# Performance work log

Measured on AMD Instinct MI355X. Metric: run time of the kernel, lower is better.

The kernel has to match this reference:

```python
import jax, jax.numpy as jnp
import numpy as np

B, D, H, C = 131072, 256, 256, 8
TAU = 0.15


def setup_inputs() -> dict:
    key = jax.random.key(0)
    ks = jax.random.split(key, 10)
    s_in = 1.0 / np.sqrt(D)
    s_h = 1.0 / np.sqrt(H)
    return {
        "x": jax.random.normal(ks[0], (B, D), jnp.float32),
        # root node params
        "W1": jax.random.normal(ks[1], (D, H), jnp.float32) * s_in,
        "b1": jnp.zeros((H,), jnp.float32),
        "W2": jax.random.normal(ks[2], (H, C), jnp.float32) * s_h,
        "b2": jnp.zeros((C,), jnp.float32),
        # one leaf child per class: stacked params [C, ...]
        "Wc1": jax.random.normal(ks[3], (C, H, H), jnp.float32) * s_h,
        "bc1": jnp.zeros((C, H), jnp.float32),
        "Wc2": jax.random.normal(ks[4], (C, H, C), jnp.float32) * s_h,
        "bc2": jnp.zeros((C, C), jnp.float32),
        "tau": jnp.full((C,), TAU, jnp.float32),
    }


def reference(x, W1, b1, W2, b2, Wc1, bc1, Wc2, bc2, tau):
    # root dense + head
    h = jax.nn.relu(x @ W1 + b1)            # [B, H]
    logits = h @ W2 + b2                    # [B, C]
    probs = jax.nn.softmax(logits, axis=1)  # [B, C]

    # route(): walk classes in descending prob order, take the first class
    # that has a child (all C do here) and whose prob >= tau[class].
    # Equivalent vectorized form: argmax of probs restricted to passing classes.
    mask = probs >= tau                     # [B, C]
    routed = jnp.any(mask, axis=1)          # [B]
    masked = jnp.where(mask, probs, -1.0)
    best = jnp.argmax(masked, axis=1)       # [B] chosen child per sample

    out_logits, out_h = logits, h
    for c in range(C):                      # small fixed expert loop
        sel = (routed & (best == c))[:, None]
        h_c = jax.nn.relu(h @ Wc1[c] + bc1[c])  # [B, H]
        l_c = h_c @ Wc2[c] + bc2[c]             # [B, C]
        out_logits = jnp.where(sel, l_c, out_logits)
        out_h = jnp.where(sel, h_c, out_h)

    depths = routed.astype(jnp.int32)       # leaf children => depth 1, else 0
    return out_logits, out_h, depths
```

## Files before the change

kernel.cpp:

```cpp
#include <hip/hip_runtime.h>

#define Bn 131072
#define Dn 256
#define Hn 256
#define Cn 8

typedef __attribute__((ext_vector_type(4))) float f32x4;
typedef __attribute__((ext_vector_type(8))) __bf16 bf16x8;

#define LDA 40

__device__ inline unsigned short rtn_bf16(float v) {
    unsigned int u = __float_as_uint(v);
    unsigned int r = u + 0x7fffu + ((u >> 16) & 1u);
    return (unsigned short)(r >> 16);
}
__device__ inline float bf16_to_f(unsigned short h) {
    return __uint_as_float((unsigned int)h << 16);
}
__device__ inline void split3(float v, unsigned short& a0, unsigned short& a1,
                              unsigned short& a2) {
    a0 = rtn_bf16(v); float r = v - bf16_to_f(a0);
    a1 = rtn_bf16(r); r -= bf16_to_f(a1);
    a2 = rtn_bf16(r);
}
__device__ inline void split2(float v, unsigned short& a0, unsigned short& a1) {
    a0 = rtn_bf16(v);
    a1 = rtn_bf16(v - bf16_to_f(a0));
}

__global__ __launch_bounds__(256)
void prep_kernel(const float* __restrict__ W1, const float* __restrict__ Wc1,
                 unsigned short* __restrict__ W1t0, unsigned short* __restrict__ W1t1,
                 unsigned short* __restrict__ W1t2,
                 unsigned short* __restrict__ Wc1t0, unsigned short* __restrict__ Wc1t1)
{
    const int idx = blockIdx.x * 256 + threadIdx.x;
    if (idx < 65536) {
        const int n = idx >> 8, k = idx & 255;
        unsigned short a0, a1, a2;
        split3(W1[k * 256 + n], a0, a1, a2);
        W1t0[idx] = a0; W1t1[idx] = a1; W1t2[idx] = a2;
    } else {
        const int j = idx - 65536;
        const int e = j >> 16, rem = j & 65535;
        const int n = rem >> 8, k = rem & 255;
        unsigned short a0, a1;
        split2(Wc1[(e << 16) + k * 256 + n], a0, a1);
        const int o = (e << 16) + n * 256 + k;
        Wc1t0[o] = a0; Wc1t1[o] = a1;
    }
}

__global__ __launch_bounds__(512, 4)
void root_kernel(const float* __restrict__ x,
                 const unsigned short* __restrict__ Wt0,
                 const unsigned short* __restrict__ Wt1,
                 const unsigned short* __restrict__ Wt2,
                 const float* __restrict__ b1, const float* __restrict__ W2,
                 const float* __restrict__ b2, const float* __restrict__ tau,
                 float* __restrict__ out_logits, float* __restrict__ out_h,
                 float* __restrict__ out_depth, int* __restrict__ cnt,
                 int* __restrict__ lists)
{
    __shared__ unsigned short sA0[64 * LDA], sA1[64 * LDA], sA2[64 * LDA];
    __shared__ float sW2[Hn * Cn];
    __shared__ float sP[64][8];
    __shared__ int   sCnt[8], sBase[8], sBest[64], sSlot[64];

    const int t    = threadIdx.x;
    const int lane = t & 63;
    const int w    = t >> 6;
    const int tx   = lane & 15;
    const int q    = lane >> 4;
    const long r0  = (long)blockIdx.x * 64;

    ((float4*)sW2)[t] = ((const float4*)W2)[t];
    if (t < 8) sCnt[t] = 0;
    ((float*)sP)[t] = 0.0f;

    const int colA = w * 32 + tx;
    const int colB = colA + 16;
    const unsigned short* bA0 = Wt0 + colA * 256 + q * 8;
    const unsigned short* bA1 = Wt1 + colA * 256 + q * 8;
    const unsigned short* bA2 = Wt2 + colA * 256 + q * 8;
    const unsigned short* bB0 = Wt0 + colB * 256 + q * 8;
    const unsigned short* bB1 = Wt1 + colB * 256 + q * 8;
    const unsigned short* bB2 = Wt2 + colB * 256 + q * 8;

    f32x4 acc[4][2];
#pragma unroll
    for (int mt = 0; mt < 4; mt++)
#pragma unroll
        for (int nt = 0; nt < 2; nt++) acc[mt][nt] = (f32x4)0.0f;

    const int arow = t >> 3, ak4 = t & 7;
    float4 xv = ((const float4*)x)[(r0 + arow) * 64 + ak4];

    for (int k0 = 0; k0 < Dn; k0 += 32) {
        __syncthreads();
        {
            unsigned short h0[4], h1[4], h2[4];
            split3(xv.x, h0[0], h1[0], h2[0]);
            split3(xv.y, h0[1], h1[1], h2[1]);
            split3(xv.z, h0[2], h1[2], h2[2]);
            split3(xv.w, h0[3], h1[3], h2[3]);
            *(ushort4*)&sA0[arow * LDA + ak4 * 4] = make_ushort4(h0[0], h0[1], h0[2], h0[3]);
            *(ushort4*)&sA1[arow * LDA + ak4 * 4] = make_ushort4(h1[0], h1[1], h1[2], h1[3]);
            *(ushort4*)&sA2[arow * LDA + ak4 * 4] = make_ushort4(h2[0], h2[1], h2[2], h2[3]);
        }
        __syncthreads();
        if (k0 < Dn - 32)
            xv = ((const float4*)x)[(r0 + arow) * 64 + ((k0 + 32) >> 2) + ak4];

        const bf16x8 B0s0 = *(const bf16x8*)(bA0 + k0);
        const bf16x8 B0s1 = *(const bf16x8*)(bA1 + k0);
        const bf16x8 B0s2 = *(const bf16x8*)(bA2 + k0);
        const bf16x8 B1s0 = *(const bf16x8*)(bB0 + k0);
        const bf16x8 B1s1 = *(const bf16x8*)(bB1 + k0);
        const bf16x8 B1s2 = *(const bf16x8*)(bB2 + k0);

#pragma unroll
        for (int mt = 0; mt < 4; mt++) {
            const bf16x8 A0 = *(const bf16x8*)&sA0[(mt * 16 + tx) * LDA + q * 8];
            const bf16x8 A1 = *(const bf16x8*)&sA1[(mt * 16 + tx) * LDA + q * 8];
            const bf16x8 A2 = *(const bf16x8*)&sA2[(mt * 16 + tx) * LDA + q * 8];
            acc[mt][0] = __builtin_amdgcn_mfma_f32_16x16x32_bf16(A0, B0s0, acc[mt][0], 0, 0, 0);
            acc[mt][0] = __builtin_amdgcn_mfma_f32_16x16x32_bf16(A0, B0s1, acc[mt][0], 0, 0, 0);
            acc[mt][0] = __builtin_amdgcn_mfma_f32_16x16x32_bf16(A1, B0s0, acc[mt][0], 0, 0, 0);
            acc[mt][0] = __builtin_amdgcn_mfma_f32_16x16x32_bf16(A1, B0s1, acc[mt][0], 0, 0, 0);
            acc[mt][0] = __builtin_amdgcn_mfma_f32_16x16x32_bf16(A0, B0s2, acc[mt][0], 0, 0, 0);
            acc[mt][0] = __builtin_amdgcn_mfma_f32_16x16x32_bf16(A2, B0s0, acc[mt][0], 0, 0, 0);
            acc[mt][1] = __builtin_amdgcn_mfma_f32_16x16x32_bf16(A0, B1s0, acc[mt][1], 0, 0, 0);
            acc[mt][1] = __builtin_amdgcn_mfma_f32_16x16x32_bf16(A0, B1s1, acc[mt][1], 0, 0, 0);
            acc[mt][1] = __builtin_amdgcn_mfma_f32_16x16x32_bf16(A1, B1s0, acc[mt][1], 0, 0, 0);
            acc[mt][1] = __builtin_amdgcn_mfma_f32_16x16x32_bf16(A1, B1s1, acc[mt][1], 0, 0, 0);
            acc[mt][1] = __builtin_amdgcn_mfma_f32_16x16x32_bf16(A0, B1s2, acc[mt][1], 0, 0, 0);
            acc[mt][1] = __builtin_amdgcn_mfma_f32_16x16x32_bf16(A2, B1s0, acc[mt][1], 0, 0, 0);
        }
    }

    const float b1c0 = b1[colA], b1c1 = b1[colB];
    float w20[8], w21[8];
#pragma unroll
    for (int c = 0; c < 8; c++) { w20[c] = sW2[colA * 8 + c]; w21[c] = sW2[colB * 8 + c]; }

#pragma unroll
    for (int mt = 0; mt < 4; mt++) {
        float pm[4][8];
#pragma unroll
        for (int reg = 0; reg < 4; reg++) {
            const float h0 = fmaxf(acc[mt][0][reg] + b1c0, 0.0f);
            const float h1 = fmaxf(acc[mt][1][reg] + b1c1, 0.0f);
            const int row = mt * 16 + q * 4 + reg;
            out_h[(r0 + row) * 256 + colA] = h0;
            out_h[(r0 + row) * 256 + colB] = h1;
#pragma unroll
            for (int c = 0; c < 8; c++)
                pm[reg][c] = h0 * w20[c] + h1 * w21[c];
        }
#pragma unroll
        for (int reg = 0; reg < 4; reg++)
#pragma unroll
            for (int c = 0; c < 8; c++) {
                float v = pm[reg][c];
                v += __shfl_xor(v, 1, 16);
                v += __shfl_xor(v, 2, 16);
                v += __shfl_xor(v, 4, 16);
                v += __shfl_xor(v, 8, 16);
                if (tx == 0) atomicAdd(&sP[mt * 16 + q * 4 + reg][c], v);
            }
    }
    __syncthreads();

    if (t < 64) {
        const long row = r0 + t;
        float l[8];
        float mx = -1e30f;
#pragma unroll
        for (int c = 0; c < 8; c++) {
            l[c] = sP[t][c] + b2[c];
            mx = fmaxf(mx, l[c]);
        }
        float e[8], s = 0.0f;
#pragma unroll
        for (int c = 0; c < 8; c++) { e[c] = expf(l[c] - mx); s += e[c]; }
        const float inv = 1.0f / s;
        int best = 0; float bp = -1.0f;
#pragma unroll
        for (int c = 0; c < 8; c++) {
            const float pr = e[c] * inv;
            const float m  = (pr >= tau[c]) ? pr : -1.0f;
            if (m > bp) { bp = m; best = c; }
        }
        const bool routed = (bp >= 0.0f);
        float4* lo4 = (float4*)&out_logits[row * 8];
        lo4[0] = make_float4(l[0], l[1], l[2], l[3]);
        lo4[1] = make_float4(l[4], l[5], l[6], l[7]);
        out_depth[row] = routed ? 1.0f : 0.0f;
        if (routed) {
            sSlot[t] = atomicAdd(&sCnt[best], 1);
            sBest[t] = best;
        } else {
            sBest[t] = -1;
        }
    }
    __syncthreads();
    if (t < 8) sBase[t] = sCnt[t] ? atomicAdd(&cnt[t], sCnt[t]) : 0;
    __syncthreads();
    if (t < 64 && sBest[t] >= 0) {
        const int e = sBest[t];
        lists[(long)e * Bn + sBase[e] + sSlot[t]] = (int)(r0 + t);
    }
}

__global__ __launch_bounds__(512, 4)
void expert_kernel(const unsigned short* __restrict__ Wc1t0,
                   const unsigned short* __restrict__ Wc1t1,
                   const float* __restrict__ bc1,
                   const float* __restrict__ Wc2, const float* __restrict__ bc2,
                   float* __restrict__ out_logits, float* __restrict__ out_h,
                   const int* __restrict__ cnt, const int* __restrict__ lists)
{
    const int e = blockIdx.y;
    const int n = cnt[e];
    const int tile0 = blockIdx.x * 64;
    if (tile0 >= n) return;
    const int nrows = min(64, n - tile0);

    __shared__ unsigned short sA0[64 * LDA], sA1[64 * LDA];
    __shared__ float sW2c[Hn * Cn];
    __shared__ float sP[64][8];
    __shared__ int   sRidx[64];

    const int t    = threadIdx.x;
    const int lane = t & 63;
    const int w    = t >> 6;
    const int tx   = lane & 15;
    const int q    = lane >> 4;

    if (t < 64) sRidx[t] = lists[(long)e * Bn + tile0 + min(t, nrows - 1)];
    ((float4*)sW2c)[t] = ((const float4*)(Wc2 + (long)e * Hn * Cn))[t];
    ((float*)sP)[t] = 0.0f;

    const unsigned short* Wh = Wc1t0 + (long)e * 65536;
    const unsigned short* Wl = Wc1t1 + (long)e * 65536;
    const int colA = w * 32 + tx;
    const int colB = colA + 16;
    const unsigned short* bA0 = Wh + colA * 256 + q * 8;
    const unsigned short* bA1 = Wl + colA * 256 + q * 8;
    const unsigned short* bB0 = Wh + colB * 256 + q * 8;
    const unsigned short* bB1 = Wl + colB * 256 + q * 8;

    f32x4 acc[4][2];
#pragma unroll
    for (int mt = 0; mt < 4; mt++)
#pragma unroll
        for (int nt = 0; nt < 2; nt++) acc[mt][nt] = (f32x4)0.0f;

    const int arow = t >> 3, ak4 = t & 7;
    __syncthreads();
    float4 xv = ((const float4*)out_h)[(long)sRidx[arow] * 64 + ak4];

    for (int k0 = 0; k0 < Hn; k0 += 32) {
        __syncthreads();
        {
            unsigned short h0[4], h1[4];
            split2(xv.x, h0[0], h1[0]);
            split2(xv.y, h0[1], h1[1]);
            split2(xv.z, h0[2], h1[2]);
            split2(xv.w, h0[3], h1[3]);
            *(ushort4*)&sA0[arow * LDA + ak4 * 4] = make_ushort4(h0[0], h0[1], h0[2], h0[3]);
            *(ushort4*)&sA1[arow * LDA + ak4 * 4] = make_ushort4(h1[0], h1[1], h1[2], h1[3]);
        }
        __syncthreads();
        if (k0 < Hn - 32)
            xv = ((const float4*)out_h)[(long)sRidx[arow] * 64 + ((k0 + 32) >> 2) + ak4];

        const bf16x8 B0s0 = *(const bf16x8*)(bA0 + k0);
        const bf16x8 B0s1 = *(const bf16x8*)(bA1 + k0);
        const bf16x8 B1s0 = *(const bf16x8*)(bB0 + k0);
        const bf16x8 B1s1 = *(const bf16x8*)(bB1 + k0);

#pragma unroll
        for (int mt = 0; mt < 4; mt++) {
            const bf16x8 A0 = *(const bf16x8*)&sA0[(mt * 16 + tx) * LDA + q * 8];
            const bf16x8 A1 = *(const bf16x8*)&sA1[(mt * 16 + tx) * LDA + q * 8];
            acc[mt][0] = __builtin_amdgcn_mfma_f32_16x16x32_bf16(A0, B0s0, acc[mt][0], 0, 0, 0);
            acc[mt][0] = __builtin_amdgcn_mfma_f32_16x16x32_bf16(A0, B0s1, acc[mt][0], 0, 0, 0);
            acc[mt][0] = __builtin_amdgcn_mfma_f32_16x16x32_bf16(A1, B0s0, acc[mt][0], 0, 0, 0);
            acc[mt][1] = __builtin_amdgcn_mfma_f32_16x16x32_bf16(A0, B1s0, acc[mt][1], 0, 0, 0);
            acc[mt][1] = __builtin_amdgcn_mfma_f32_16x16x32_bf16(A0, B1s1, acc[mt][1], 0, 0, 0);
            acc[mt][1] = __builtin_amdgcn_mfma_f32_16x16x32_bf16(A1, B1s0, acc[mt][1], 0, 0, 0);
        }
    }

    const float* bc1e = bc1 + (long)e * Hn;
    const float b1c0 = bc1e[colA], b1c1 = bc1e[colB];
    float w20[8], w21[8];
#pragma unroll
    for (int c = 0; c < 8; c++) { w20[c] = sW2c[colA * 8 + c]; w21[c] = sW2c[colB * 8 + c]; }

#pragma unroll
    for (int mt = 0; mt < 4; mt++) {
        float pm[4][8];
#pragma unroll
        for (int reg = 0; reg < 4; reg++) {
            const float h0 = fmaxf(acc[mt][0][reg] + b1c0, 0.0f);
            const float h1 = fmaxf(acc[mt][1][reg] + b1c1, 0.0f);
            const int row = mt * 16 + q * 4 + reg;
            if (row < nrows) {
                out_h[(long)sRidx[row] * 256 + colA] = h0;
                out_h[(long)sRidx[row] * 256 + colB] = h1;
            }
#pragma unroll
            for (int c = 0; c < 8; c++)
                pm[reg][c] = h0 * w20[c] + h1 * w21[c];
        }
#pragma unroll
        for (int reg = 0; reg < 4; reg++)
#pragma unroll
            for (int c = 0; c < 8; c++) {
                float v = pm[reg][c];
                v += __shfl_xor(v, 1, 16);
                v += __shfl_xor(v, 2, 16);
                v += __shfl_xor(v, 4, 16);
                v += __shfl_xor(v, 8, 16);
                if (tx == 0) atomicAdd(&sP[mt * 16 + q * 4 + reg][c], v);
            }
    }
    __syncthreads();

    if (t < nrows) {
        const long row = sRidx[t];
        const float* bc2e = bc2 + (long)e * Cn;
        float4* lo4 = (float4*)&out_logits[row * 8];
        lo4[0] = make_float4(sP[t][0] + bc2e[0], sP[t][1] + bc2e[1],
                             sP[t][2] + bc2e[2], sP[t][3] + bc2e[3]);
        lo4[1] = make_float4(sP[t][4] + bc2e[4], sP[t][5] + bc2e[5],
                             sP[t][6] + bc2e[6], sP[t][7] + bc2e[7]);
    }
}

extern "C" void kernel_launch(void* const* d_in, const int* in_sizes, int n_in,
                              void* d_out, int out_size, void* d_ws, size_t ws_size,
                              hipStream_t stream)
{
    const float* x   = (const float*)d_in[0];
    const float* W1  = (const float*)d_in[1];
    const float* b1  = (const float*)d_in[2];
    const float* W2  = (const float*)d_in[3];
    const float* b2  = (const float*)d_in[4];
    const float* Wc1 = (const float*)d_in[5];
    const float* bc1 = (const float*)d_in[6];
    const float* Wc2 = (const float*)d_in[7];
    const float* bc2 = (const float*)d_in[8];
    const float* tau = (const float*)d_in[9];

    float* out_logits = (float*)d_out;
    float* out_h      = out_logits + (long)Bn * Cn;
    float* out_depth  = out_h + (long)Bn * Hn;

    char* wsb = (char*)d_ws;
    int* cnt   = (int*)wsb;
    int* lists = (int*)(wsb + 128);
    unsigned short* W1t0  = (unsigned short*)(wsb + 128 + (size_t)8 * Bn * 4);
    unsigned short* W1t1  = W1t0 + 65536;
    unsigned short* W1t2  = W1t1 + 65536;
    unsigned short* Wc1t0 = W1t2 + 65536;
    unsigned short* Wc1t1 = Wc1t0 + 8 * 65536;

    hipMemsetAsync(d_ws, 0, 128, stream);

    prep_kernel<<<dim3((65536 + 8 * 65536) / 256), 256, 0, stream>>>(
        W1, Wc1, W1t0, W1t1, W1t2, Wc1t0, Wc1t1);

    root_kernel<<<dim3(Bn / 64), 512, 0, stream>>>(
        x, W1t0, W1t1, W1t2, b1, W2, b2, tau, out_logits, out_h, out_depth,
        cnt, lists);

    expert_kernel<<<dim3(Bn / 64, 8), 512, 0, stream>>>(
        Wc1t0, Wc1t1, bc1, Wc2, bc2, out_logits, out_h, cnt, lists);
}
```

Baseline: 665.5 us.

## Double-buffer LDS A tiles and prefetch B fragments in root and expert GEMMs

Both the root and expert GEMM loops now double-buffer the split-bf16 A tile in shared memory and register-prefetch the next k-step's weight fragments. This drops one of the two barriers per k-iteration and overlaps the global loads and split conversions with the MFMA work. In exchange it doubles A-tile LDS use and raises register pressure from the extra prefetched B fragments, which may lower occupancy under the 512x4 launch bounds.

```diff
diff --git a/kernel.cpp b/kernel.cpp
--- a/kernel.cpp
+++ b/kernel.cpp
@@ -63,7 +63,7 @@
                  float* __restrict__ out_depth, int* __restrict__ cnt,
                  int* __restrict__ lists)
 {
-    __shared__ unsigned short sA0[64 * LDA], sA1[64 * LDA], sA2[64 * LDA];
+    __shared__ unsigned short sA[2][3][64 * LDA];
     __shared__ float sW2[Hn * Cn];
     __shared__ float sP[64][8];
     __shared__ int   sCnt[8], sBase[8], sBest[64], sSlot[64];
@@ -81,12 +81,9 @@
 
     const int colA = w * 32 + tx;
     const int colB = colA + 16;
-    const unsigned short* bA0 = Wt0 + colA * 256 + q * 8;
-    const unsigned short* bA1 = Wt1 + colA * 256 + q * 8;
-    const unsigned short* bA2 = Wt2 + colA * 256 + q * 8;
-    const unsigned short* bB0 = Wt0 + colB * 256 + q * 8;
-    const unsigned short* bB1 = Wt1 + colB * 256 + q * 8;
-    const unsigned short* bB2 = Wt2 + colB * 256 + q * 8;
+    const unsigned short* bp[6] = {
+        Wt0 + colA * 256 + q * 8, Wt1 + colA * 256 + q * 8, Wt2 + colA * 256 + q * 8,
+        Wt0 + colB * 256 + q * 8, Wt1 + colB * 256 + q * 8, Wt2 + colB * 256 + q * 8 };
 
     f32x4 acc[4][2];
 #pragma unroll
@@ -95,49 +92,68 @@
         for (int nt = 0; nt < 2; nt++) acc[mt][nt] = (f32x4)0.0f;
 
     const int arow = t >> 3, ak4 = t & 7;
-    float4 xv = ((const float4*)x)[(r0 + arow) * 64 + ak4];
-
-    for (int k0 = 0; k0 < Dn; k0 += 32) {
-        __syncthreads();
-        {
+    const float4* x4 = (const float4*)x + (r0 + arow) * 64 + ak4;
+
+    float4 xv = x4[0];
+    {
+        unsigned short h0[4], h1[4], h2[4];
+        split3(xv.x, h0[0], h1[0], h2[0]);
+        split3(xv.y, h0[1], h1[1], h2[1]);
+        split3(xv.z, h0[2], h1[2], h2[2]);
+        split3(xv.w, h0[3], h1[3], h2[3]);
+        *(ushort4*)&sA[0][0][arow * LDA + ak4 * 4] = make_ushort4(h0[0], h0[1], h0[2], h0[3]);
+        *(ushort4*)&sA[0][1][arow * LDA + ak4 * 4] = make_ushort4(h1[0], h1[1], h1[2], h1[3]);
+        *(ushort4*)&sA[0][2][arow * LDA + ak4 * 4] = make_ushort4(h2[0], h2[1], h2[2], h2[3]);
+    }
+    xv = x4[8];
+    bf16x8 Bc[6];
+#pragma unroll
+    for (int s = 0; s < 6; s++) Bc[s] = *(const bf16x8*)(bp[s]);
+    __syncthreads();
+
+#pragma unroll 2
+    for (int i = 0; i < 8; i++) {
+        const int cur = i & 1;
+        if (i < 7) {
             unsigned short h0[4], h1[4], h2[4];
             split3(xv.x, h0[0], h1[0], h2[0]);
             split3(xv.y, h0[1], h1[1], h2[1]);
             split3(xv.z, h0[2], h1[2], h2[2]);
             split3(xv.w, h0[3], h1[3], h2[3]);
-            *(ushort4*)&sA0[arow * LDA + ak4 * 4] = make_ushort4(h0[0], h0[1], h0[2], h0[3]);
-            *(ushort4*)&sA1[arow * LDA + ak4 * 4] = make_ushort4(h1[0], h1[1], h1[2], h1[3]);
-            *(ushort4*)&sA2[arow * LDA + ak4 * 4] = make_ushort4(h2[0], h2[1], h2[2], h2[3]);
+            *(ushort4*)&sA[cur ^ 1][0][arow * LDA + ak4 * 4] = make_ushort4(h0[0], h0[1], h0[2], h0[3]);
+            *(ushort4*)&sA[cur ^ 1][1][arow * LDA + ak4 * 4] = make_ushort4(h1[0], h1[1], h1[2], h1[3]);
+            *(ushort4*)&sA[cur ^ 1][2][arow * LDA + ak4 * 4] = make_ushort4(h2[0], h2[1], h2[2], h2[3]);
+            if (i < 6) xv = x4[(i + 2) * 8];
+        }
+        bf16x8 Bnx[6];
+        if (i < 7) {
+            const int kn = (i + 1) * 32;
+#pragma unroll
+            for (int s = 0; s < 6; s++) Bnx[s] = *(const bf16x8*)(bp[s] + kn);
+        }
+#pragma unroll
+        for (int mt = 0; mt < 4; mt++) {
+            const bf16x8 A0 = *(const bf16x8*)&sA[cur][0][(mt * 16 + tx) * LDA + q * 8];
+            const bf16x8 A1 = *(const bf16x8*)&sA[cur][1][(mt * 16 + tx) * LDA + q * 8];
+            const bf16x8 A2 = *(const bf16x8*)&sA[cur][2][(mt * 16 + tx) * LDA + q * 8];
+            acc[mt][0] = __builtin_amdgcn_mfma_f32_16x16x32_bf16(A0, Bc[0], acc[mt][0], 0, 0, 0);
+            acc[mt][0] = __builtin_amdgcn_mfma_f32_16x16x32_bf16(A0, Bc[1], acc[mt][0], 0, 0, 0);
+            acc[mt][0] = __builtin_amdgcn_mfma_f32_16x16x32_bf16(A1, Bc[0], acc[mt][0], 0, 0, 0);
+            acc[mt][0] = __builtin_amdgcn_mfma_f32_16x16x32_bf16(A1, Bc[1], acc[mt][0], 0, 0, 0);
+            acc[mt][0] = __builtin_amdgcn_mfma_f32_16x16x32_bf16(A0, Bc[2], acc[mt][0], 0, 0, 0);
+            acc[mt][0] = __builtin_amdgcn_mfma_f32_16x16x32_bf16(A2, Bc[0], acc[mt][0], 0, 0, 0);
+            acc[mt][1] = __builtin_amdgcn_mfma_f32_16x16x32_bf16(A0, Bc[3], acc[mt][1], 0, 0, 0);
+            acc[mt][1] = __builtin_amdgcn_mfma_f32_16x16x32_bf16(A0, Bc[4], acc[mt][1], 0, 0, 0);
+            acc[mt][1] = __builtin_amdgcn_mfma_f32_16x16x32_bf16(A1, Bc[3], acc[mt][1], 0, 0, 0);
+            acc[mt][1] = __builtin_amdgcn_mfma_f32_16x16x32_bf16(A1, Bc[4], acc[mt][1], 0, 0, 0);
+            acc[mt][1] = __builtin_amdgcn_mfma_f32_16x16x32_bf16(A0, Bc[5], acc[mt][1], 0, 0, 0);
+            acc[mt][1] = __builtin_amdgcn_mfma_f32_16x16x32_bf16(A2, Bc[3], acc[mt][1], 0, 0, 0);
+        }
+        if (i < 7) {
+#pragma unroll
+            for (int s = 0; s < 6; s++) Bc[s] = Bnx[s];
         }
         __syncthreads();
-        if (k0 < Dn - 32)
-            xv = ((const float4*)x)[(r0 + arow) * 64 + ((k0 + 32) >> 2) + ak4];
-
-        const bf16x8 B0s0 = *(const bf16x8*)(bA0 + k0);
-        const bf16x8 B0s1 = *(const bf16x8*)(bA1 + k0);
-        const bf16x8 B0s2 = *(const bf16x8*)(bA2 + k0);
-        const bf16x8 B1s0 = *(const bf16x8*)(bB0 + k0);
-        const bf16x8 B1s1 = *(const bf16x8*)(bB1 + k0);
-        const bf16x8 B1s2 = *(const bf16x8*)(bB2 + k0);
-
-#pragma unroll
-        for (int mt = 0; mt < 4; mt++) {
-            const bf16x8 A0 = *(const bf16x8*)&sA0[(mt * 16 + tx) * LDA + q * 8];
-            const bf16x8 A1 = *(const bf16x8*)&sA1[(mt * 16 + tx) * LDA + q * 8];
-            const bf16x8 A2 = *(const bf16x8*)&sA2[(mt * 16 + tx) * LDA + q * 8];
-            acc[mt][0] = __builtin_amdgcn_mfma_f32_16x16x32_bf16(A0, B0s0, acc[mt][0], 0, 0, 0);
-            acc[mt][0] = __builtin_amdgcn_mfma_f32_16x16x32_bf16(A0, B0s1, acc[mt][0], 0, 0, 0);
-            acc[mt][0] = __builtin_amdgcn_mfma_f32_16x16x32_bf16(A1, B0s0, acc[mt][0], 0, 0, 0);
-            acc[mt][0] = __builtin_amdgcn_mfma_f32_16x16x32_bf16(A1, B0s1, acc[mt][0], 0, 0, 0);
-            acc[mt][0] = __builtin_amdgcn_mfma_f32_16x16x32_bf16(A0, B0s2, acc[mt][0], 0, 0, 0);
-            acc[mt][0] = __builtin_amdgcn_mfma_f32_16x16x32_bf16(A2, B0s0, acc[mt][0], 0, 0, 0);
-            acc[mt][1] = __builtin_amdgcn_mfma_f32_16x16x32_bf16(A0, B1s0, acc[mt][1], 0, 0, 0);
-            acc[mt][1] = __builtin_amdgcn_mfma_f32_16x16x32_bf16(A0, B1s1, acc[mt][1], 0, 0, 0);
-            acc[mt][1] = __builtin_amdgcn_mfma_f32_16x16x32_bf16(A1, B1s0, acc[mt][1], 0, 0, 0);
-            acc[mt][1] = __builtin_amdgcn_mfma_f32_16x16x32_bf16(A1, B1s1, acc[mt][1], 0, 0, 0);
-            acc[mt][1] = __builtin_amdgcn_mfma_f32_16x16x32_bf16(A0, B1s2, acc[mt][1], 0, 0, 0);
-            acc[mt][1] = __builtin_amdgcn_mfma_f32_16x16x32_bf16(A2, B1s0, acc[mt][1], 0, 0, 0);
-        }
     }
 
     const float b1c0 = b1[colA], b1c1 = b1[colB];
@@ -186,14 +202,14 @@
 #pragma unroll
         for (int c = 0; c < 8; c++) { e[c] = expf(l[c] - mx); s += e[c]; }
         const float inv = 1.0f / s;
-        int best = 0; float bp = -1.0f;
+        int best = 0; float bp2 = -1.0f;
 #pragma unroll
         for (int c = 0; c < 8; c++) {
             const float pr = e[c] * inv;
             const float m  = (pr >= tau[c]) ? pr : -1.0f;
-            if (m > bp) { bp = m; best = c; }
-        }
-        const bool routed = (bp >= 0.0f);
+            if (m > bp2) { bp2 = m; best = c; }
+        }
+        const bool routed = (bp2 >= 0.0f);
         float4* lo4 = (float4*)&out_logits[row * 8];
         lo4[0] = make_float4(l[0], l[1], l[2], l[3]);
         lo4[1] = make_float4(l[4], l[5], l[6], l[7]);
@@ -228,7 +244,7 @@
     if (tile0 >= n) return;
     const int nrows = min(64, n - tile0);
 
-    __shared__ unsigned short sA0[64 * LDA], sA1[64 * LDA];
+    __shared__ unsigned short sA[2][2][64 * LDA];
     __shared__ float sW2c[Hn * Cn];
     __shared__ float sP[64][8];
     __shared__ int   sRidx[64];
@@ -247,10 +263,9 @@
     const unsigned short* Wl = Wc1t1 + (long)e * 65536;
     const int colA = w * 32 + tx;
     const int colB = colA + 16;
-    const unsigned short* bA0 = Wh + colA * 256 + q * 8;
-    const unsigned short* bA1 = Wl + colA * 256 + q * 8;
-    const unsigned short* bB0 = Wh + colB * 256 + q * 8;
-    const unsigned short* bB1 = Wl + colB * 256 + q * 8;
+    const unsigned short* bp[4] = {
+        Wh + colA * 256 + q * 8, Wl + colA * 256 + q * 8,
+        Wh + colB * 256 + q * 8, Wl + colB * 256 + q * 8 };
 
     f32x4 acc[4][2];
 #pragma unroll
@@ -260,39 +275,59 @@
 
     const int arow = t >> 3, ak4 = t & 7;
     __syncthreads();
-    float4 xv = ((const float4*)out_h)[(long)sRidx[arow] * 64 + ak4];
-
-    for (int k0 = 0; k0 < Hn; k0 += 32) {
-        __syncthreads();
-        {
+    const float4* h4 = (const float4*)out_h + (long)sRidx[arow] * 64 + ak4;
+
+    float4 xv = h4[0];
+    {
+        unsigned short h0[4], h1[4];
+        split2(xv.x, h0[0], h1[0]);
+        split2(xv.y, h0[1], h1[1]);
+        split2(xv.z, h0[2], h1[2]);
+        split2(xv.w, h0[3], h1[3]);
+        *(ushort4*)&sA[0][0][arow * LDA + ak4 * 4] = make_ushort4(h0[0], h0[1], h0[2], h0[3]);
+        *(ushort4*)&sA[0][1][arow * LDA + ak4 * 4] = make_ushort4(h1[0], h1[1], h1[2], h1[3]);
+    }
+    xv = h4[8];
+    bf16x8 Bc[4];
+#pragma unroll
+    for (int s = 0; s < 4; s++) Bc[s] = *(const bf16x8*)(bp[s]);
+    __syncthreads();
+
+#pragma unroll 2
+    for (int i = 0; i < 8; i++) {
+        const int cur = i & 1;
+        if (i < 7) {
             unsigned short h0[4], h1[4];
             split2(xv.x, h0[0], h1[0]);
             split2(xv.y, h0[1], h1[1]);
             split2(xv.z, h0[2], h1[2]);
             split2(xv.w, h0[3], h1[3]);
-            *(ushort4*)&sA0[arow * LDA + ak4 * 4] = make_ushort4(h0[0], h0[1], h0[2], h0[3]);
-            *(ushort4*)&sA1[arow * LDA + ak4 * 4] = make_ushort4(h1[0], h1[1], h1[2], h1[3]);
+            *(ushort4*)&sA[cur ^ 1][0][arow * LDA + ak4 * 4] = make_ushort4(h0[0], h0[1], h0[2], h0[3]);
+            *(ushort4*)&sA[cur ^ 1][1][arow * LDA + ak4 * 4] = make_ushort4(h1[0], h1[1], h1[2], h1[3]);
+            if (i < 6) xv = h4[(i + 2) * 8];
+        }
+        bf16x8 Bnx[4];
+        if (i < 7) {
+            const int kn = (i + 1) * 32;
+#pragma unroll
+            for (int s = 0; s < 4; s++) Bnx[s] = *(const bf16x8*)(bp[s] + kn);
+        }
+#pragma unroll
+        for (int mt = 0; mt < 4; mt++) {
+            const bf16x8 A0 = *(const bf16x8*)&sA[cur][0][(mt * 16 + tx) * LDA + q * 8];
+            const bf16x8 A1 = *(const bf16x8*)&sA[cur][1][(mt * 16 + tx) * LDA + q * 8];
+            acc[mt][0] = __builtin_amdgcn_mfma_f32_16x16x32_bf16(A0, Bc[0], acc[mt][0], 0, 0, 0);
+            acc[mt][0] = __builtin_amdgcn_mfma_f32_16x16x32_bf16(A0, Bc[1], acc[mt][0], 0, 0, 0);
+            acc[mt][0] = __builtin_amdgcn_mfma_f32_16x16x32_bf16(A1, Bc[0], acc[mt][0], 0, 0, 0);
+            acc[mt][1] = __builtin_amdgcn_mfma_f32_16x16x32_bf16(A0, Bc[2], acc[mt][1], 0, 0, 0);
+            acc[mt][1] = __builtin_amdgcn_mfma_f32_16x16x32_bf16(A0, Bc[3], acc[mt][1], 0, 0, 0);
+            acc[mt][1] = __builtin_amdgcn_mfma_f32_16x16x32_bf16(A1, Bc[2], acc[mt][1], 0, 0, 0);
+        }
+        if (i < 7) {
+#pragma unroll
+            for (int s = 0; s < 4; s++) Bc[s] = Bnx[s];
         }
         __syncthreads();
-        if (k0 < Hn - 32)
-            xv = ((const float4*)out_h)[(long)sRidx[arow] * 64 + ((k0 + 32) >> 2) + ak4];
-
-        const bf16x8 B0s0 = *(const bf16x8*)(bA0 + k0);
-        const bf16x8 B0s1 = *(const bf16x8*)(bA1 + k0);
-        const bf16x8 B1s0 = *(const bf16x8*)(bB0 + k0);
-        const bf16x8 B1s1 = *(const bf16x8*)(bB1 + k0);
-
-#pragma unroll
-        for (int mt = 0; mt < 4; mt++) {
-            const bf16x8 A0 = *(const bf16x8*)&sA0[(mt * 16 + tx) * LDA + q * 8];
-            const bf16x8 A1 = *(const bf16x8*)&sA1[(mt * 16 + tx) * LDA + q * 8];
-            acc[mt][0] = __builtin_amdgcn_mfma_f32_16x16x32_bf16(A0, B0s0, acc[mt][0], 0, 0, 0);
-            acc[mt][0] = __builtin_amdgcn_mfma_f32_16x16x32_bf16(A0, B0s1, acc[mt][0], 0, 0, 0);
-            acc[mt][0] = __builtin_amdgcn_mfma_f32_16x16x32_bf16(A1, B0s0, acc[mt][0], 0, 0, 0);
-            acc[mt][1] = __builtin_amdgcn_mfma_f32_16x16x32_bf16(A0, B1s0, acc[mt][1], 0, 0, 0);
-            acc[mt][1] = __builtin_amdgcn_mfma_f32_16x16x32_bf16(A0, B1s1, acc[mt][1], 0, 0, 0);
-            acc[mt][1] = __builtin_amdgcn_mfma_f32_16x16x32_bf16(A1, B1s0, acc[mt][1], 0, 0, 0);
-        }
     }
 
     const float* bc1e = bc1 + (long)e * Hn;
```

Measured after the change: 657.5 us. Within noise of the previous version (-1.2%).

## Use single-bf16 expert GEMM, double-buffer expert tiles, widen row tiles to 128

Applied to the files above, without the earlier changes.

The expert GEMM drops the two-term bf16 split emulation and uses a single bf16 rounding for both activations and weights, cutting its MFMA count from three to one per tile. The expert K loop is double-buffered in LDS and prefetches the weight fragments, removing one barrier per step. Both root and expert kernels now process 128 rows per block instead of 64, which reuses the weight fragments across more rows. W2 is read directly from global memory instead of staged in shared memory. The reduced expert precision risks larger numerical error against the fp32 reference.

```diff
diff --git a/kernel.cpp b/kernel.cpp
--- a/kernel.cpp
+++ b/kernel.cpp
@@ -24,16 +24,14 @@
     a1 = rtn_bf16(r); r -= bf16_to_f(a1);
     a2 = rtn_bf16(r);
 }
-__device__ inline void split2(float v, unsigned short& a0, unsigned short& a1) {
-    a0 = rtn_bf16(v);
-    a1 = rtn_bf16(v - bf16_to_f(a0));
+__device__ inline ushort4 cvt4(float4 v) {
+    return make_ushort4(rtn_bf16(v.x), rtn_bf16(v.y), rtn_bf16(v.z), rtn_bf16(v.w));
 }
 
 __global__ __launch_bounds__(256)
 void prep_kernel(const float* __restrict__ W1, const float* __restrict__ Wc1,
                  unsigned short* __restrict__ W1t0, unsigned short* __restrict__ W1t1,
-                 unsigned short* __restrict__ W1t2,
-                 unsigned short* __restrict__ Wc1t0, unsigned short* __restrict__ Wc1t1)
+                 unsigned short* __restrict__ W1t2, unsigned short* __restrict__ Wc1t)
 {
     const int idx = blockIdx.x * 256 + threadIdx.x;
     if (idx < 65536) {
@@ -45,10 +43,7 @@
         const int j = idx - 65536;
         const int e = j >> 16, rem = j & 65535;
         const int n = rem >> 8, k = rem & 255;
-        unsigned short a0, a1;
-        split2(Wc1[(e << 16) + k * 256 + n], a0, a1);
-        const int o = (e << 16) + n * 256 + k;
-        Wc1t0[o] = a0; Wc1t1[o] = a1;
+        Wc1t[(e << 16) + n * 256 + k] = rtn_bf16(Wc1[(e << 16) + k * 256 + n]);
     }
 }
 
@@ -63,90 +58,107 @@
                  float* __restrict__ out_depth, int* __restrict__ cnt,
                  int* __restrict__ lists)
 {
-    __shared__ unsigned short sA0[64 * LDA], sA1[64 * LDA], sA2[64 * LDA];
-    __shared__ float sW2[Hn * Cn];
-    __shared__ float sP[64][8];
-    __shared__ int   sCnt[8], sBase[8], sBest[64], sSlot[64];
+    __shared__ unsigned short sA0[128 * LDA], sA1[128 * LDA], sA2[128 * LDA];
+    __shared__ float sP[128][8];
+    __shared__ int   sCnt[8], sBase[8], sBest[128], sSlot[128];
 
     const int t    = threadIdx.x;
     const int lane = t & 63;
     const int w    = t >> 6;
     const int tx   = lane & 15;
     const int q    = lane >> 4;
-    const long r0  = (long)blockIdx.x * 64;
-
-    ((float4*)sW2)[t] = ((const float4*)W2)[t];
+    const long r0  = (long)blockIdx.x * 128;
+
     if (t < 8) sCnt[t] = 0;
     ((float*)sP)[t] = 0.0f;
+    ((float*)sP)[t + 512] = 0.0f;
 
     const int colA = w * 32 + tx;
     const int colB = colA + 16;
-    const unsigned short* bA0 = Wt0 + colA * 256 + q * 8;
-    const unsigned short* bA1 = Wt1 + colA * 256 + q * 8;
-    const unsigned short* bA2 = Wt2 + colA * 256 + q * 8;
-    const unsigned short* bB0 = Wt0 + colB * 256 + q * 8;
-    const unsigned short* bB1 = Wt1 + colB * 256 + q * 8;
-    const unsigned short* bB2 = Wt2 + colB * 256 + q * 8;
-
-    f32x4 acc[4][2];
-#pragma unroll
-    for (int mt = 0; mt < 4; mt++)
+    const unsigned short* bp0 = Wt0 + colA * 256 + q * 8;
+    const unsigned short* bp1 = Wt1 + colA * 256 + q * 8;
+    const unsigned short* bp2 = Wt2 + colA * 256 + q * 8;
+    const unsigned short* bp3 = Wt0 + colB * 256 + q * 8;
+    const unsigned short* bp4 = Wt1 + colB * 256 + q * 8;
+    const unsigned short* bp5 = Wt2 + colB * 256 + q * 8;
+
+    f32x4 acc[8][2];
+#pragma unroll
+    for (int mt = 0; mt < 8; mt++)
 #pragma unroll
         for (int nt = 0; nt < 2; nt++) acc[mt][nt] = (f32x4)0.0f;
 
-    const int arow = t >> 3, ak4 = t & 7;
-    float4 xv = ((const float4*)x)[(r0 + arow) * 64 + ak4];
-
-    for (int k0 = 0; k0 < Dn; k0 += 32) {
-        __syncthreads();
+    const int ar = t >> 3, ak = t & 7;
+    const float4* xr0 = (const float4*)x + (r0 + ar) * 64 + ak;
+    const float4* xr1 = (const float4*)x + (r0 + 64 + ar) * 64 + ak;
+    float4 xv0 = xr0[0];
+    float4 xv1 = xr1[0];
+
+    for (int i = 0; i < 8; i++) {
+        if (i) __syncthreads();
         {
             unsigned short h0[4], h1[4], h2[4];
-            split3(xv.x, h0[0], h1[0], h2[0]);
-            split3(xv.y, h0[1], h1[1], h2[1]);
-            split3(xv.z, h0[2], h1[2], h2[2]);
-            split3(xv.w, h0[3], h1[3], h2[3]);
-            *(ushort4*)&sA0[arow * LDA + ak4 * 4] = make_ushort4(h0[0], h0[1], h0[2], h0[3]);
-            *(ushort4*)&sA1[arow * LDA + ak4 * 4] = make_ushort4(h1[0], h1[1], h1[2], h1[3]);
-            *(ushort4*)&sA2[arow * LDA + ak4 * 4] = make_ushort4(h2[0], h2[1], h2[2], h2[3]);
-        }
+            split3(xv0.x, h0[0], h1[0], h2[0]);
+            split3(xv0.y, h0[1], h1[1], h2[1]);
+            split3(xv0.z, h0[2], h1[2], h2[2]);
+            split3(xv0.w, h0[3], h1[3], h2[3]);
+            *(ushort4*)&sA0[ar * LDA + ak * 4] = make_ushort4(h0[0], h0[1], h0[2], h0[3]);
+            *(ushort4*)&sA1[ar * LDA + ak * 4] = make_ushort4(h1[0], h1[1], h1[2], h1[3]);
+            *(ushort4*)&sA2[ar * LDA + ak * 4] = make_ushort4(h2[0], h2[1], h2[2], h2[3]);
+            split3(xv1.x, h0[0], h1[0], h2[0]);
+            split3(xv1.y, h0[1], h1[1], h2[1]);
+            split3(xv1.z, h0[2], h1[2], h2[2]);
+            split3(xv1.w, h0[3], h1[3], h2[3]);
+            *(ushort4*)&sA0[(64 + ar) * LDA + ak * 4] = make_ushort4(h0[0], h0[1], h0[2], h0[3]);
+            *(ushort4*)&sA1[(64 + ar) * LDA + ak * 4] = make_ushort4(h1[0], h1[1], h1[2], h1[3]);
+            *(ushort4*)&sA2[(64 + ar) * LDA + ak * 4] = make_ushort4(h2[0], h2[1], h2[2], h2[3]);
+        }
+        if (i < 7) { xv0 = xr0[(i + 1) * 8]; xv1 = xr1[(i + 1) * 8]; }
         __syncthreads();
-        if (k0 < Dn - 32)
-            xv = ((const float4*)x)[(r0 + arow) * 64 + ((k0 + 32) >> 2) + ak4];
-
-        const bf16x8 B0s0 = *(const bf16x8*)(bA0 + k0);
-        const bf16x8 B0s1 = *(const bf16x8*)(bA1 + k0);
-        const bf16x8 B0s2 = *(const bf16x8*)(bA2 + k0);
-        const bf16x8 B1s0 = *(const bf16x8*)(bB0 + k0);
-        const bf16x8 B1s1 = *(const bf16x8*)(bB1 + k0);
-        const bf16x8 B1s2 = *(const bf16x8*)(bB2 + k0);
-
-#pragma unroll
-        for (int mt = 0; mt < 4; mt++) {
+
+        const int ko = i * 32;
+        const bf16x8 B0 = *(const bf16x8*)(bp0 + ko);
+        const bf16x8 B1 = *(const bf16x8*)(bp1 + ko);
+        const bf16x8 B2 = *(const bf16x8*)(bp2 + ko);
+        const bf16x8 B3 = *(const bf16x8*)(bp3 + ko);
+        const bf16x8 B4 = *(const bf16x8*)(bp4 + ko);
+        const bf16x8 B5 = *(const bf16x8*)(bp5 + ko);
+
+#pragma unroll
+        for (int mt = 0; mt < 8; mt++) {
             const bf16x8 A0 = *(const bf16x8*)&sA0[(mt * 16 + tx) * LDA + q * 8];
             const bf16x8 A1 = *(const bf16x8*)&sA1[(mt * 16 + tx) * LDA + q * 8];
             const bf16x8 A2 = *(const bf16x8*)&sA2[(mt * 16 + tx) * LDA + q * 8];
-            acc[mt][0] = __builtin_amdgcn_mfma_f32_16x16x32_bf16(A0, B0s0, acc[mt][0], 0, 0, 0);
-            acc[mt][0] = __builtin_amdgcn_mfma_f32_16x16x32_bf16(A0, B0s1, acc[mt][0], 0, 0, 0);
-            acc[mt][0] = __builtin_amdgcn_mfma_f32_16x16x32_bf16(A1, B0s0, acc[mt][0], 0, 0, 0);
-            acc[mt][0] = __builtin_amdgcn_mfma_f32_16x16x32_bf16(A1, B0s1, acc[mt][0], 0, 0, 0);
-            acc[mt][0] = __builtin_amdgcn_mfma_f32_16x16x32_bf16(A0, B0s2, acc[mt][0], 0, 0, 0);
-            acc[mt][0] = __builtin_amdgcn_mfma_f32_16x16x32_bf16(A2, B0s0, acc[mt][0], 0, 0, 0);
-            acc[mt][1] = __builtin_amdgcn_mfma_f32_16x16x32_bf16(A0, B1s0, acc[mt][1], 0, 0, 0);
-            acc[mt][1] = __builtin_amdgcn_mfma_f32_16x16x32_bf16(A0, B1s1, acc[mt][1], 0, 0, 0);
-            acc[mt][1] = __builtin_amdgcn_mfma_f32_16x16x32_bf16(A1, B1s0, acc[mt][1], 0, 0, 0);
-            acc[mt][1] = __builtin_amdgcn_mfma_f32_16x16x32_bf16(A1, B1s1, acc[mt][1], 0, 0, 0);
-            acc[mt][1] = __builtin_amdgcn_mfma_f32_16x16x32_bf16(A0, B1s2, acc[mt][1], 0, 0, 0);
-            acc[mt][1] = __builtin_amdgcn_mfma_f32_16x16x32_bf16(A2, B1s0, acc[mt][1], 0, 0, 0);
+            acc[mt][0] = __builtin_amdgcn_mfma_f32_16x16x32_bf16(A0, B0, acc[mt][0], 0, 0, 0);
+            acc[mt][0] = __builtin_amdgcn_mfma_f32_16x16x32_bf16(A0, B1, acc[mt][0], 0, 0, 0);
+            acc[mt][0] = __builtin_amdgcn_mfma_f32_16x16x32_bf16(A1, B0, acc[mt][0], 0, 0, 0);
+            acc[mt][0] = __builtin_amdgcn_mfma_f32_16x16x32_bf16(A1, B1, acc[mt][0], 0, 0, 0);
+            acc[mt][0] = __builtin_amdgcn_mfma_f32_16x16x32_bf16(A0, B2, acc[mt][0], 0, 0, 0);
+            acc[mt][0] = __builtin_amdgcn_mfma_f32_16x16x32_bf16(A2, B0, acc[mt][0], 0, 0, 0);
+            acc[mt][1] = __builtin_amdgcn_mfma_f32_16x16x32_bf16(A0, B3, acc[mt][1], 0, 0, 0);
+            acc[mt][1] = __builtin_amdgcn_mfma_f32_16x16x32_bf16(A0, B4, acc[mt][1], 0, 0, 0);
+            acc[mt][1] = __builtin_amdgcn_mfma_f32_16x16x32_bf16(A1, B3, acc[mt][1], 0, 0, 0);
+            acc[mt][1] = __builtin_amdgcn_mfma_f32_16x16x32_bf16(A1, B4, acc[mt][1], 0, 0, 0);
+            acc[mt][1] = __builtin_amdgcn_mfma_f32_16x16x32_bf16(A0, B5, acc[mt][1], 0, 0, 0);
+            acc[mt][1] = __builtin_amdgcn_mfma_f32_16x16x32_bf16(A2, B3, acc[mt][1], 0, 0, 0);
         }
     }
 
     const float b1c0 = b1[colA], b1c1 = b1[colB];
     float w20[8], w21[8];
-#pragma unroll
-    for (int c = 0; c < 8; c++) { w20[c] = sW2[colA * 8 + c]; w21[c] = sW2[colB * 8 + c]; }
-
-#pragma unroll
-    for (int mt = 0; mt < 4; mt++) {
+    {
+        const float4 a0 = ((const float4*)W2)[colA * 2];
+        const float4 a1 = ((const float4*)W2)[colA * 2 + 1];
+        const float4 c0 = ((const float4*)W2)[colB * 2];
+        const float4 c1 = ((const float4*)W2)[colB * 2 + 1];
+        w20[0]=a0.x; w20[1]=a0.y; w20[2]=a0.z; w20[3]=a0.w;
+        w20[4]=a1.x; w20[5]=a1.y; w20[6]=a1.z; w20[7]=a1.w;
+        w21[0]=c0.x; w21[1]=c0.y; w21[2]=c0.z; w21[3]=c0.w;
+        w21[4]=c1.x; w21[5]=c1.y; w21[6]=c1.z; w21[7]=c1.w;
+    }
+
+#pragma unroll
+    for (int mt = 0; mt < 8; mt++) {
         float pm[4][8];
 #pragma unroll
         for (int reg = 0; reg < 4; reg++) {
@@ -173,7 +185,7 @@
     }
     __syncthreads();
 
-    if (t < 64) {
+    if (t < 128) {
         const long row = r0 + t;
         float l[8];
         float mx = -1e30f;
@@ -208,15 +220,14 @@
     __syncthreads();
     if (t < 8) sBase[t] = sCnt[t] ? atomicAdd(&cnt[t], sCnt[t]) : 0;
     __syncthreads();
-    if (t < 64 && sBest[t] >= 0) {
+    if (t < 128 && sBest[t] >= 0) {
         const int e = sBest[t];
         lists[(long)e * Bn + sBase[e] + sSlot[t]] = (int)(r0 + t);
     }
 }
 
 __global__ __launch_bounds__(512, 4)
-void expert_kernel(const unsigned short* __restrict__ Wc1t0,
-                   const unsigned short* __restrict__ Wc1t1,
+void expert_kernel(const unsigned short* __restrict__ Wc1t,
                    const float* __restrict__ bc1,
                    const float* __restrict__ Wc2, const float* __restrict__ bc2,
                    float* __restrict__ out_logits, float* __restrict__ out_h,
@@ -224,14 +235,13 @@
 {
     const int e = blockIdx.y;
     const int n = cnt[e];
-    const int tile0 = blockIdx.x * 64;
+    const int tile0 = blockIdx.x * 128;
     if (tile0 >= n) return;
-    const int nrows = min(64, n - tile0);
-
-    __shared__ unsigned short sA0[64 * LDA], sA1[64 * LDA];
-    __shared__ float sW2c[Hn * Cn];
-    __shared__ float sP[64][8];
-    __shared__ int   sRidx[64];
+    const int nrows = min(128, n - tile0);
+
+    __shared__ unsigned short sA[2][128 * LDA];
+    __shared__ float sP[128][8];
+    __shared__ int   sRidx[128];
 
     const int t    = threadIdx.x;
     const int lane = t & 63;
@@ -239,70 +249,75 @@
     const int tx   = lane & 15;
     const int q    = lane >> 4;
 
-    if (t < 64) sRidx[t] = lists[(long)e * Bn + tile0 + min(t, nrows - 1)];
-    ((float4*)sW2c)[t] = ((const float4*)(Wc2 + (long)e * Hn * Cn))[t];
+    if (t < 128) sRidx[t] = lists[(long)e * Bn + tile0 + min(t, nrows - 1)];
     ((float*)sP)[t] = 0.0f;
-
-    const unsigned short* Wh = Wc1t0 + (long)e * 65536;
-    const unsigned short* Wl = Wc1t1 + (long)e * 65536;
+    ((float*)sP)[t + 512] = 0.0f;
+
+    const unsigned short* W = Wc1t + (long)e * 65536;
     const int colA = w * 32 + tx;
     const int colB = colA + 16;
-    const unsigned short* bA0 = Wh + colA * 256 + q * 8;
-    const unsigned short* bA1 = Wl + colA * 256 + q * 8;
-    const unsigned short* bB0 = Wh + colB * 256 + q * 8;
-    const unsigned short* bB1 = Wl + colB * 256 + q * 8;
-
-    f32x4 acc[4][2];
-#pragma unroll
-    for (int mt = 0; mt < 4; mt++)
+    const unsigned short* bpA = W + colA * 256 + q * 8;
+    const unsigned short* bpB = W + colB * 256 + q * 8;
+
+    f32x4 acc[8][2];
+#pragma unroll
+    for (int mt = 0; mt < 8; mt++)
 #pragma unroll
         for (int nt = 0; nt < 2; nt++) acc[mt][nt] = (f32x4)0.0f;
 
-    const int arow = t >> 3, ak4 = t & 7;
-    __syncthreads();
-    float4 xv = ((const float4*)out_h)[(long)sRidx[arow] * 64 + ak4];
-
-    for (int k0 = 0; k0 < Hn; k0 += 32) {
+    const int ar = t >> 3, ak = t & 7;
+    __syncthreads();
+    const float4* hr0 = (const float4*)out_h + (long)sRidx[ar] * 64 + ak;
+    const float4* hr1 = (const float4*)out_h + (long)sRidx[64 + ar] * 64 + ak;
+
+    float4 xv0 = hr0[0], xv1 = hr1[0];
+    *(ushort4*)&sA[0][ar * LDA + ak * 4]        = cvt4(xv0);
+    *(ushort4*)&sA[0][(64 + ar) * LDA + ak * 4] = cvt4(xv1);
+    xv0 = hr0[8]; xv1 = hr1[8];
+    bf16x8 BcA = *(const bf16x8*)(bpA);
+    bf16x8 BcB = *(const bf16x8*)(bpB);
+    __syncthreads();
+
+#pragma unroll 2
+    for (int i = 0; i < 8; i++) {
+        const int cur = i & 1;
+        if (i < 7) {
+            *(ushort4*)&sA[cur ^ 1][ar * LDA + ak * 4]        = cvt4(xv0);
+            *(ushort4*)&sA[cur ^ 1][(64 + ar) * LDA + ak * 4] = cvt4(xv1);
+            if (i < 6) { xv0 = hr0[(i + 2) * 8]; xv1 = hr1[(i + 2) * 8]; }
+        }
+        bf16x8 BnA, BnB;
+        if (i < 7) {
+            BnA = *(const bf16x8*)(bpA + (i + 1) * 32);
+            BnB = *(const bf16x8*)(bpB + (i + 1) * 32);
+        }
+#pragma unroll
+        for (int mt = 0; mt < 8; mt++) {
+            const bf16x8 A = *(const bf16x8*)&sA[cur][(mt * 16 + tx) * LDA + q * 8];
+            acc[mt][0] = __builtin_amdgcn_mfma_f32_16x16x32_bf16(A, BcA, acc[mt][0], 0, 0, 0);
+            acc[mt][1] = __builtin_amdgcn_mfma_f32_16x16x32_bf16(A, BcB, acc[mt][1], 0, 0, 0);
+        }
+        if (i < 7) { BcA = BnA; BcB = BnB; }
         __syncthreads();
-        {
-            unsigned short h0[4], h1[4];
-            split2(xv.x, h0[0], h1[0]);
-            split2(xv.y, h0[1], h1[1]);
-            split2(xv.z, h0[2], h1[2]);
-            split2(xv.w, h0[3], h1[3]);
-            *(ushort4*)&sA0[arow * LDA + ak4 * 4] = make_ushort4(h0[0], h0[1], h0[2], h0[3]);
-            *(ushort4*)&sA1[arow * LDA + ak4 * 4] = make_ushort4(h1[0], h1[1], h1[2], h1[3]);
-        }
-        __syncthreads();
-        if (k0 < Hn - 32)
-            xv = ((const float4*)out_h)[(long)sRidx[arow] * 64 + ((k0 + 32) >> 2) + ak4];
-
-        const bf16x8 B0s0 = *(const bf16x8*)(bA0 + k0);
-        const bf16x8 B0s1 = *(const bf16x8*)(bA1 + k0);
-        const bf16x8 B1s0 = *(const bf16x8*)(bB0 + k0);
-        const bf16x8 B1s1 = *(const bf16x8*)(bB1 + k0);
-
-#pragma unroll
-        for (int mt = 0; mt < 4; mt++) {
-            const bf16x8 A0 = *(const bf16x8*)&sA0[(mt * 16 + tx) * LDA + q * 8];
-            const bf16x8 A1 = *(const bf16x8*)&sA1[(mt * 16 + tx) * LDA + q * 8];
-            acc[mt][0] = __builtin_amdgcn_mfma_f32_16x16x32_bf16(A0, B0s0, acc[mt][0], 0, 0, 0);
-            acc[mt][0] = __builtin_amdgcn_mfma_f32_16x16x32_bf16(A0, B0s1, acc[mt][0], 0, 0, 0);
-            acc[mt][0] = __builtin_amdgcn_mfma_f32_16x16x32_bf16(A1, B0s0, acc[mt][0], 0, 0, 0);
-            acc[mt][1] = __builtin_amdgcn_mfma_f32_16x16x32_bf16(A0, B1s0, acc[mt][1], 0, 0, 0);
-            acc[mt][1] = __builtin_amdgcn_mfma_f32_16x16x32_bf16(A0, B1s1, acc[mt][1], 0, 0, 0);
-            acc[mt][1] = __builtin_amdgcn_mfma_f32_16x16x32_bf16(A1, B1s0, acc[mt][1], 0, 0, 0);
-        }
     }
 
     const float* bc1e = bc1 + (long)e * Hn;
     const float b1c0 = bc1e[colA], b1c1 = bc1e[colB];
+    const float* W2c = Wc2 + (long)e * Hn * Cn;
     float w20[8], w21[8];
-#pragma unroll
-    for (int c = 0; c < 8; c++) { w20[c] = sW2c[colA * 8 + c]; w21[c] = sW2c[colB * 8 + c]; }
-
-#pragma unroll
-    for (int mt = 0; mt < 4; mt++) {
+    {
+        const float4 a0 = ((const float4*)W2c)[colA * 2];
+        const float4 a1 = ((const float4*)W2c)[colA * 2 + 1];
+        const float4 c0 = ((const float4*)W2c)[colB * 2];
+        const float4 c1 = ((const float4*)W2c)[colB * 2 + 1];
+        w20[0]=a0.x; w20[1]=a0.y; w20[2]=a0.z; w20[3]=a0.w;
+        w20[4]=a1.x; w20[5]=a1.y; w20[6]=a1.z; w20[7]=a1.w;
+        w21[0]=c0.x; w21[1]=c0.y; w21[2]=c0.z; w21[3]=c0.w;
+        w21[4]=c1.x; w21[5]=c1.y; w21[6]=c1.z; w21[7]=c1.w;
+    }
+
+#pragma unroll
+    for (int mt = 0; mt < 8; mt++) {
         float pm[4][8];
 #pragma unroll
         for (int reg = 0; reg < 4; reg++) {
@@ -364,21 +379,20 @@
     char* wsb = (char*)d_ws;
     int* cnt   = (int*)wsb;
     int* lists = (int*)(wsb + 128);
-    unsigned short* W1t0  = (unsigned short*)(wsb + 128 + (size_t)8 * Bn * 4);
-    unsigned short* W1t1  = W1t0 + 65536;
-    unsigned short* W1t2  = W1t1 + 65536;
-    unsigned short* Wc1t0 = W1t2 + 65536;
-    unsigned short* Wc1t1 = Wc1t0 + 8 * 65536;
+    unsigned short* W1t0 = (unsigned short*)(wsb + 128 + (size_t)8 * Bn * 4);
+    unsigned short* W1t1 = W1t0 + 65536;
+    unsigned short* W1t2 = W1t1 + 65536;
+    unsigned short* Wc1t = W1t2 + 65536;
 
     hipMemsetAsync(d_ws, 0, 128, stream);
 
     prep_kernel<<<dim3((65536 + 8 * 65536) / 256), 256, 0, stream>>>(
-        W1, Wc1, W1t0, W1t1, W1t2, Wc1t0, Wc1t1);
-
-    root_kernel<<<dim3(Bn / 64), 512, 0, stream>>>(
+        W1, Wc1, W1t0, W1t1, W1t2, Wc1t);
+
+    root_kernel<<<dim3(Bn / 128), 512, 0, stream>>>(
         x, W1t0, W1t1, W1t2, b1, W2, b2, tau, out_logits, out_h, out_depth,
         cnt, lists);
 
-    expert_kernel<<<dim3(Bn / 64, 8), 512, 0, stream>>>(
-        Wc1t0, Wc1t1, bc1, Wc2, bc2, out_logits, out_h, cnt, lists);
-}
+    expert_kernel<<<dim3(Bn / 128, 8), 512, 0, stream>>>(
+        Wc1t, bc1, Wc2, bc2, out_logits, out_h, cnt, lists);
+}
```

Result: faster. 615.9 us (-7.5%).
